# Performance work log

Measured on AMD Instinct MI355X. Metric: run time of the kernel, lower is better.

Reference implementation:

```python
import jax, jax.numpy as jnp
import numpy as np

V_SIZE, E, H = 30000, 256, 128   # vocab, emb_dim, GRU hidden per direction
B, U, T, ND = 32, 32, 128, 64    # dialogues, utterances, max tokens, dialogue-id table size
SCALE = E ** 0.5                  # attention normalise_factor = hid_size**0.5, hid_size = emb_dim


def _gru_dir(x_seq, w_ih, w_hh, b_ih, b_hh):
    """Unidirectional torch-style GRU. x_seq: [N,T,E] -> [N,T,H]."""
    xp = jnp.einsum('nte,ge->ntg', x_seq, w_ih) + b_ih   # precompute input gates [N,T,3H]
    xp = jnp.swapaxes(xp, 0, 1)                          # [T,N,3H]

    def step(h, xpt):
        gh = h @ w_hh.T + b_hh
        r = jax.nn.sigmoid(xpt[:, :H] + gh[:, :H])
        z = jax.nn.sigmoid(xpt[:, H:2 * H] + gh[:, H:2 * H])
        n = jnp.tanh(xpt[:, 2 * H:] + r * gh[:, 2 * H:])
        h_new = (1.0 - z) * n + z * h
        return h_new, h_new

    h0 = jnp.zeros((x_seq.shape[0], H), x_seq.dtype)
    _, out = jax.lax.scan(step, h0, xp)
    return jnp.swapaxes(out, 0, 1)


def _forward(x, d_ids, utt_len, emb_table,
             w_ih_f, w_hh_f, b_ih_f, b_hh_f,
             w_ih_b, w_hh_b, b_ih_b, b_hh_b,
             wq, bq, wk, bk, wv, bv, wo, bo, wl, bl):
    b, u, t = x.shape
    N = b * u
    emb = emb_table[x.reshape(N, t)]                      # [N,T,E]
    lens = jnp.clip(utt_len[d_ids].reshape(N), 1, t)      # valid tokens per utterance
    pos = jnp.arange(t)
    # index map that reverses the valid prefix (padding region clipped, unused)
    rev_idx = jnp.clip(lens[:, None] - 1 - pos[None, :], 0, t - 1)  # [N,T]

    o_f = _gru_dir(emb, w_ih_f, w_hh_f, b_ih_f, b_hh_f)   # causal => correct on valid prefix
    emb_rev = jnp.take_along_axis(emb, rev_idx[:, :, None], axis=1)
    o_b = jnp.take_along_axis(_gru_dir(emb_rev, w_ih_b, w_hh_b, b_ih_b, b_hh_b),
                              rev_idx[:, :, None], axis=1)
    h = jnp.concatenate([o_f, o_b], axis=-1)              # [N,T,E] bi-GRU states

    # self-attention pooling; original takes op[-1], so only the query at the
    # last valid token (lens-1) is needed -- identical math, less compute.
    k = jnp.einsum('nte,he->nth', h, wk) + bk
    v = jnp.einsum('nte,he->nth', h, wv) + bv
    h_last = jnp.take_along_axis(h, (lens - 1)[:, None, None], axis=1)[:, 0]  # [N,E]
    q = h_last @ wq.T + bq
    score = jnp.einsum('nh,nth->nt', q, k) / SCALE
    score = jnp.where(pos[None, :] < lens[:, None], score, -jnp.inf)
    attn = jax.nn.softmax(score, axis=-1)
    ctx = jnp.einsum('nt,nth->nh', attn, v)
    out = (ctx @ wo.T + bo) @ wl.T + bl                   # make_output then final linear
    return out.reshape(b, u, -1)


def setup_inputs() -> dict:
    key = jax.random.key(0)
    ks = jax.random.split(key, 16)

    def p(k, shape):
        return (jax.random.normal(k, shape, jnp.float32) / np.sqrt(shape[-1])).astype(jnp.float32)

    return {
        'x': jax.random.randint(ks[0], (B, U, T), 0, V_SIZE, dtype=jnp.int32),
        'd_ids': jax.random.randint(ks[1], (B,), 0, ND, dtype=jnp.int32),
        'utt_len': jax.random.randint(ks[2], (ND, U), 1, T + 1, dtype=jnp.int32),
        'emb_table': p(ks[3], (V_SIZE, E)),
        'w_ih_f': p(ks[4], (3 * H, E)), 'w_hh_f': p(ks[5], (3 * H, H)),
        'b_ih_f': jnp.zeros(3 * H, jnp.float32), 'b_hh_f': jnp.zeros(3 * H, jnp.float32),
        'w_ih_b': p(ks[6], (3 * H, E)), 'w_hh_b': p(ks[7], (3 * H, H)),
        'b_ih_b': jnp.zeros(3 * H, jnp.float32), 'b_hh_b': jnp.zeros(3 * H, jnp.float32),
        'wq': p(ks[8], (E, E)), 'bq': jnp.zeros(E, jnp.float32),
        'wk': p(ks[9], (E, E)), 'bk': jnp.zeros(E, jnp.float32),
        'wv': p(ks[10], (E, E)), 'bv': jnp.zeros(E, jnp.float32),
        'wo': p(ks[11], (E, E)), 'bo': jnp.zeros(E, jnp.float32),
        'wl': p(ks[12], (E, E)), 'bl': jnp.zeros(E, jnp.float32),
    }


def reference(x, d_ids, utt_len, emb_table,
              w_ih_f, w_hh_f, b_ih_f, b_hh_f,
              w_ih_b, w_hh_b, b_ih_b, b_hh_b,
              wq, bq, wk, bk, wv, bv, wo, bo, wl, bl):
    return _forward(x, d_ids, utt_len, emb_table,
                    w_ih_f, w_hh_f, b_ih_f, b_hh_f,
                    w_ih_b, w_hh_b, b_ih_b, b_hh_b,
                    wq, bq, wk, bk, wv, bv, wo, bo, wl, bl)
```

## Files before the change

### kernel.cpp

```cpp
#include <hip/hip_runtime.h>
#include <hip/hip_bf16.h>
#include <math.h>
#include <stdint.h>

typedef unsigned short u16;
typedef unsigned int   u32;
typedef __attribute__((ext_vector_type(8))) short bf16x8;
typedef __attribute__((ext_vector_type(4))) float f32x4;

#define EDIM 256
#define HDIM 128
#define TLEN 128
#define NUTT 1024
#define UU   32
#define NBU  8

#define WS_FLAG 0
#define WS_LENS 64
#define WS_TAB  4608
#define WS_COPY 8192
#define WS_OF   18874368LL
#define WS_OB   52428800LL

#define MFMA16(a, b, c) __builtin_amdgcn_mfma_f32_16x16x32_bf16((a), (b), (c), 0, 0, 0)
#define SOUT(u, s, j) ((u) * 1096 + (s) * 136 + (j))

__constant__ int G_SZ[18] = {7680000, 98304, 49152, 384, 384, 98304, 49152, 384, 384,
                             65536, 256, 65536, 65536, 256, 65536, 256, 65536, 256};

__device__ __forceinline__ float b2f(u16 b) {
    u32 u = ((u32)b) << 16; float f; __builtin_memcpy(&f, &u, 4); return f;
}
__device__ __forceinline__ u16 f2b(float f) {
    u32 u; __builtin_memcpy(&u, &f, 4);
    u32 r = u + 0x7FFFu + ((u >> 16) & 1u);
    return (u16)(r >> 16);
}
__device__ __forceinline__ u16 f2b_hw(float f) {
    __hip_bfloat16 h = __float2bfloat16(f);
    u16 v; __builtin_memcpy(&v, &h, 2); return v;
}
__device__ __forceinline__ float fsigmoid(float x) { return 1.0f / (1.0f + __expf(-x)); }
__device__ __forceinline__ float ftanh(float x) { return 1.0f - 2.0f / (__expf(2.0f * x) + 1.0f); }

__global__ __launch_bounds__(256)
void k_convert(void* ws,
               const int* __restrict__ d_ids, const int* __restrict__ utt_len,
               const void* a0, const void* a1, const void* a2, const void* a3,
               const void* a4, const void* a5, const void* a6, const void* a7,
               const void* a8, const void* a9, const void* a10, const void* a11,
               const void* a12, const void* a13, const void* a14, const void* a15,
               const void* a16, const void* a17) {
    __shared__ int scnt[4];
    const int tid = threadIdx.x, lane = tid & 63, wid = tid >> 6;
    const u16* p = (const u16*)a0;
    int cnt = 0;
#pragma unroll 8
    for (int i = tid; i < 16384; i += 256)
        cnt += ((p[i] & 0x7F80) == 0x7F80) ? 1 : 0;
#pragma unroll
    for (int o = 32; o > 0; o >>= 1) cnt += __shfl_down(cnt, o);
    if (lane == 0) scnt[wid] = cnt;
    __syncthreads();
    const int flag = (scnt[0] + scnt[1] + scnt[2] + scnt[3] > 0) ? 1 : 0;

    if (blockIdx.x == 0) {
        if (tid == 0) {
            const void* orig[18] = {a0,a1,a2,a3,a4,a5,a6,a7,a8,a9,a10,a11,a12,a13,a14,a15,a16,a17};
            *(int*)((char*)ws + WS_FLAG) = flag;
            const u16** tab = (const u16**)((char*)ws + WS_TAB);
            char* base = (char*)ws + WS_COPY;
            long long cum = 0;
            for (int a = 0; a < 18; ++a) {
                tab[a] = flag ? (const u16*)(base + cum * 2) : (const u16*)orig[a];
                cum += G_SZ[a];
            }
        }
        int* lens = (int*)((char*)ws + WS_LENS);
#pragma unroll 4
        for (int n = tid; n < NUTT; n += 256) {
            int b = n >> 5;
            int u = n & (UU - 1);
            int L = utt_len[d_ids[b] * UU + u];
            lens[n] = min(max(L, 1), TLEN);
        }
    }

    if (flag == 0) return;
    const void* orig[18] = {a0,a1,a2,a3,a4,a5,a6,a7,a8,a9,a10,a11,a12,a13,a14,a15,a16,a17};
    u16* base = (u16*)((char*)ws + WS_COPY);
    const int gtid = blockIdx.x * blockDim.x + tid;
    const int gs   = gridDim.x * blockDim.x;
    long long cum = 0;
    for (int a = 0; a < 18; ++a) {
        const float4* src = (const float4*)orig[a];
        uint2* dst = (uint2*)(base + cum);
        const int n4 = G_SZ[a] >> 2;
        for (int i = gtid; i < n4; i += gs) {
            float4 v = src[i];
            uint2 pk;
            pk.x = (u32)f2b(v.x) | ((u32)f2b(v.y) << 16);
            pk.y = (u32)f2b(v.z) | ((u32)f2b(v.w) << 16);
            dst[i] = pk;
        }
        cum += G_SZ[a];
    }
}

__global__ __launch_bounds__(512)
void k_scan(const int* __restrict__ x, void* ws) {
    const u16* const* tab = (const u16* const*)((char*)ws + WS_TAB);
    const int dir = blockIdx.y;
    const u16* emb  = tab[0];
    const u16* w_ih = tab[1 + dir * 4];
    const u16* w_hh = tab[2 + dir * 4];
    const u16* b_ih = tab[3 + dir * 4];
    const u16* b_hh = tab[4 + dir * 4];
    u16* outp = (u16*)((char*)ws + (dir ? WS_OB : WS_OF));
    const int* lens = (const int*)((char*)ws + WS_LENS);

    const int n0 = blockIdx.x * NBU;
    __shared__ __align__(16) u16 sh_emb[2][NBU][264];
    __shared__ __align__(16) u16 sh_hi[2][NBU * 136];
    __shared__ __align__(16) u16 sh_lo[2][NBU * 136];
    __shared__ __align__(16) u16 sh_out[2][NBU * 1096];
    __shared__ int sh_tok[NBU * 132];
    __shared__ int sh_L[NBU];

    const int tid = threadIdx.x, lane = tid & 63, wvi = tid >> 6;
    const int q4 = lane >> 4, mm = lane & 15;
    const int j = wvi * 16 + mm;
    const int u8 = mm & 7;
    const int arr0 = (q4 & 2);
    const bool a2 = (arr0 != 0);
    const bool lo32 = (lane < 32);

    for (int i = tid; i < NBU * 136; i += 512) { sh_hi[0][i] = 0; sh_lo[0][i] = 0; }
    for (int i = tid; i < NBU * TLEN; i += 512) {
        const int u = i >> 7, tt = i & 127;
        sh_tok[u * 132 + tt] = x[(n0 + u) * TLEN + tt];
    }
    if (tid < NBU) sh_L[tid] = lens[n0 + tid];

    bf16x8 wih[3][8]; bf16x8 whh[3][4];
    float bcr, bcz, bxn, bgn;
#pragma unroll
    for (int n3 = 0; n3 < 3; ++n3) {
        const int g = n3 * HDIM + j;
#pragma unroll
        for (int ks = 0; ks < 8; ++ks)
            wih[n3][ks] = *(const bf16x8*)(w_ih + g * EDIM + ks * 32 + q4 * 8);
#pragma unroll
        for (int ks = 0; ks < 4; ++ks)
            whh[n3][ks] = *(const bf16x8*)(w_hh + g * HDIM + ks * 32 + q4 * 8);
    }
    bcr = b2f(b_ih[j]) + b2f(b_hh[j]);
    bcz = b2f(b_ih[HDIM + j]) + b2f(b_hh[HDIM + j]);
    bxn = b2f(b_ih[2 * HDIM + j]);
    bgn = b2f(b_hh[2 * HDIM + j]);

    float hprev[2] = {0.f, 0.f};
    const f32x4 zero4 = {0.f, 0.f, 0.f, 0.f};
    __syncthreads();

    int Lm = sh_L[0];
#pragma unroll
    for (int u = 1; u < NBU; ++u) Lm = max(Lm, sh_L[u]);
    const int tmax = (Lm + 7) & ~7;

    const int pf_u = lane & 7;
    const int pf_c = (wvi & 3) * 8 + (lane >> 3);
    const int pf_L = sh_L[pf_u];
    const int tsel = wvi >> 2;

    {
        const int te = dir ? max(pf_L - 1 - tsel, 0) : tsel;
        const int tok = sh_tok[pf_u * 132 + te];
        uint4 v = *(const uint4*)(emb + (size_t)tok * EDIM + pf_c * 8);
        *(uint4*)&sh_emb[tsel][pf_u][pf_c * 8] = v;
    }
    __syncthreads();

    for (int t0 = 0; t0 < tmax; t0 += 2) {
        const int obuf = (t0 >> 3) & 1;
        const bool more = (t0 + 2 < tmax);

        uint4 pf;
        if (more) {
            const int tt = t0 + 2 + tsel;
            const int te = dir ? max(pf_L - 1 - tt, 0) : tt;
            const int tok = sh_tok[pf_u * 132 + te];
            pf = *(const uint4*)(emb + (size_t)tok * EDIM + pf_c * 8);
        }

        f32x4 accx[3];
        {
            const u16* eb_ = (mm < 8) ? &sh_emb[0][u8][0] : &sh_emb[1][u8][0];
            bf16x8 a = *(const bf16x8*)(eb_ + q4 * 8);
            accx[0] = MFMA16(a, wih[0][0], zero4);
            accx[1] = MFMA16(a, wih[1][0], zero4);
            accx[2] = MFMA16(a, wih[2][0], zero4);
#pragma unroll
            for (int ks = 1; ks < 8; ++ks) {
                bf16x8 av = *(const bf16x8*)(eb_ + ks * 32 + q4 * 8);
                accx[0] = MFMA16(av, wih[0][ks], accx[0]);
                accx[1] = MFMA16(av, wih[1][ks], accx[1]);
                accx[2] = MFMA16(av, wih[2][ks], accx[2]);
            }
        }
        float xA[3][2], xB[3][2];
#pragma unroll
        for (int g = 0; g < 3; ++g) {
#pragma unroll
            for (int r = 0; r < 2; ++r) {
                const float sv = a2 ? accx[g][r] : accx[g][2 + r];
                const float ov = a2 ? accx[g][2 + r] : accx[g][r];
                const float pv = __shfl_xor(sv, 32);
                xA[g][r] = lo32 ? ov : pv;
                xB[g][r] = lo32 ? pv : ov;
            }
        }

        {
            f32x4 accg[3];
            const u16* hb_ = ((mm < 8) ? sh_hi[0] : sh_lo[0]) + u8 * 136;
            {
                bf16x8 a = *(const bf16x8*)(hb_ + q4 * 8);
                accg[0] = MFMA16(a, whh[0][0], zero4);
                accg[1] = MFMA16(a, whh[1][0], zero4);
                accg[2] = MFMA16(a, whh[2][0], zero4);
            }
#pragma unroll
            for (int ks = 1; ks < 4; ++ks) {
                bf16x8 a = *(const bf16x8*)(hb_ + ks * 32 + q4 * 8);
                accg[0] = MFMA16(a, whh[0][ks], accg[0]);
                accg[1] = MFMA16(a, whh[1][ks], accg[1]);
                accg[2] = MFMA16(a, whh[2][ks], accg[2]);
            }
            const int slot = t0 & 7;
#pragma unroll
            for (int r = 0; r < 2; ++r) {
                float gg[3];
#pragma unroll
                for (int g = 0; g < 3; ++g) {
                    const float sv = a2 ? accg[g][r] : accg[g][2 + r];
                    const float ov = a2 ? accg[g][2 + r] : accg[g][r];
                    gg[g] = ov + __shfl_xor(sv, 32);
                }
                const int u = (q4 * 4 + arr0 + r) & 7;
                const float rg = fsigmoid(xA[0][r] + gg[0] + bcr);
                const float zg = fsigmoid(xA[1][r] + gg[1] + bcz);
                const float nn = ftanh((xA[2][r] + bxn) + rg * (gg[2] + bgn));
                const float hn = (1.0f - zg) * nn + zg * hprev[r];
                hprev[r] = hn;
                const u16 hb16 = f2b_hw(hn);
                sh_hi[1][u * 136 + j] = hb16;
                sh_lo[1][u * 136 + j] = f2b_hw(hn - b2f(hb16));
                sh_out[obuf][SOUT(u, slot, j)] = hb16;
            }
        }
        __syncthreads();

        {
            f32x4 accg[3];
            const u16* hb_ = ((mm < 8) ? sh_hi[1] : sh_lo[1]) + u8 * 136;
            {
                bf16x8 a = *(const bf16x8*)(hb_ + q4 * 8);
                accg[0] = MFMA16(a, whh[0][0], zero4);
                accg[1] = MFMA16(a, whh[1][0], zero4);
                accg[2] = MFMA16(a, whh[2][0], zero4);
            }
#pragma unroll
            for (int ks = 1; ks < 4; ++ks) {
                bf16x8 a = *(const bf16x8*)(hb_ + ks * 32 + q4 * 8);
                accg[0] = MFMA16(a, whh[0][ks], accg[0]);
                accg[1] = MFMA16(a, whh[1][ks], accg[1]);
                accg[2] = MFMA16(a, whh[2][ks], accg[2]);
            }
            const int slot = (t0 & 7) + 1;
#pragma unroll
            for (int r = 0; r < 2; ++r) {
                float gg[3];
#pragma unroll
                for (int g = 0; g < 3; ++g) {
                    const float sv = a2 ? accg[g][r] : accg[g][2 + r];
                    const float ov = a2 ? accg[g][2 + r] : accg[g][r];
                    gg[g] = ov + __shfl_xor(sv, 32);
                }
                const int u = (q4 * 4 + arr0 + r) & 7;
                const float rg = fsigmoid(xB[0][r] + gg[0] + bcr);
                const float zg = fsigmoid(xB[1][r] + gg[1] + bcz);
                const float nn = ftanh((xB[2][r] + bxn) + rg * (gg[2] + bgn));
                const float hn = (1.0f - zg) * nn + zg * hprev[r];
                hprev[r] = hn;
                const u16 hb16 = f2b_hw(hn);
                sh_hi[0][u * 136 + j] = hb16;
                sh_lo[0][u * 136 + j] = f2b_hw(hn - b2f(hb16));
                sh_out[obuf][SOUT(u, slot, j)] = hb16;
            }
        }
        if (more)
            *(uint4*)&sh_emb[tsel][pf_u][pf_c * 8] = pf;
        __syncthreads();

        if (((t0 + 1) & 7) == 7) {
            const int rowIdx = tid >> 3;
            const int part   = tid & 7;
            const int fu = rowIdx >> 3, fs = rowIdx & 7;
            const int tt = ((t0 + 1) & ~7) + fs;
            const int tout = dir ? (sh_L[fu] - 1 - tt) : tt;
            if (tout >= 0) {
                const u16* srcp = &sh_out[obuf][SOUT(fu, fs, part * 16)];
                uint4 v0 = *(const uint4*)(srcp);
                uint4 v1 = *(const uint4*)(srcp + 8);
                u16* dstp = outp + ((size_t)(n0 + fu) * TLEN + tout) * HDIM + part * 16;
                *(uint4*)(dstp)     = v0;
                *(uint4*)(dstp + 8) = v1;
            }
        }
    }
}

__global__ __launch_bounds__(256)
void k_attn(void* ws, void* outv) {
    const u16* const* tab = (const u16* const*)((char*)ws + WS_TAB);
    const u16* wq = tab[9];  const u16* bq = tab[10];
    const u16* wk = tab[11];
    const u16* wv = tab[12]; const u16* bv = tab[13];
    const u16* wo = tab[14]; const u16* bo = tab[15];
    const u16* wl = tab[16]; const u16* bl = tab[17];
    const int* lens = (const int*)((char*)ws + WS_LENS);
    const int flag = *(const int*)((const char*)ws + WS_FLAG);

    const int n = blockIdx.x;
    const int L = lens[n];
    const u16* hf = (const u16*)((char*)ws + WS_OF) + (size_t)n * TLEN * HDIM;
    const u16* hb = (const u16*)((char*)ws + WS_OB) + (size_t)n * TLEN * HDIM;

    __shared__ float sh_hl[EDIM];
    __shared__ float sh_v1[EDIM];
    __shared__ float sh_uv[EDIM];
    __shared__ float sh_a[4 * EDIM];
    __shared__ float sh_m[4], sh_l[4];

    const int tid = threadIdx.x, lane = tid & 63, wid = tid >> 6;

    sh_hl[tid] = (tid < HDIM) ? b2f(hf[(size_t)(L - 1) * HDIM + tid])
                              : b2f(hb[(size_t)(L - 1) * HDIM + (tid - HDIM)]);
    __syncthreads();

    {
        float s0 = b2f(bq[tid]), s1 = 0.0f;
        const u16* wr = wq + tid * EDIM;
#pragma unroll
        for (int ks = 0; ks < 32; ks += 2) {
            bf16x8 w8 = *(const bf16x8*)(wr + ks * 8);
            bf16x8 w9 = *(const bf16x8*)(wr + ks * 8 + 8);
#pragma unroll
            for (int d = 0; d < 8; ++d) {
                s0 += b2f((u16)w8[d]) * sh_hl[ks * 8 + d];
                s1 += b2f((u16)w9[d]) * sh_hl[ks * 8 + 8 + d];
            }
        }
        sh_v1[tid] = s0 + s1;
    }
    __syncthreads();

    {
        float s0 = 0.0f, s1 = 0.0f;
        for (int i = 0; i < EDIM; i += 2) {
            s0 += b2f(wk[i * EDIM + tid]) * sh_v1[i];
            s1 += b2f(wk[(i + 1) * EDIM + tid]) * sh_v1[i + 1];
        }
        sh_uv[tid] = s0 + s1;
    }
    __syncthreads();

    {
        const int e0 = lane * 4;
        const float u0 = sh_uv[e0], u1 = sh_uv[e0 + 1];
        const float u2 = sh_uv[e0 + 2], u3 = sh_uv[e0 + 3];
        float m = -1e30f, l = 0.0f;
        float a0 = 0.f, a1 = 0.f, a2 = 0.f, a3 = 0.f;
        for (int t = wid; t < L; t += 4) {
            const u16* src = (lane < 32) ? (hf + (size_t)t * HDIM + lane * 4)
                                         : (hb + (size_t)t * HDIM + (lane - 32) * 4);
            uint2 pv = *(const uint2*)src;
            const float h0 = b2f((u16)(pv.x & 0xFFFF));
            const float h1 = b2f((u16)(pv.x >> 16));
            const float h2 = b2f((u16)(pv.y & 0xFFFF));
            const float h3 = b2f((u16)(pv.y >> 16));
            float p = h0 * u0 + h1 * u1 + h2 * u2 + h3 * u3;
#pragma unroll
            for (int o = 32; o > 0; o >>= 1) p += __shfl_xor(p, o);
            const float s = p * 0.0625f;
            const float mn = fmaxf(m, s);
            const float c = __expf(m - mn);
            const float w = __expf(s - mn);
            l = l * c + w;
            a0 = a0 * c + w * h0;
            a1 = a1 * c + w * h1;
            a2 = a2 * c + w * h2;
            a3 = a3 * c + w * h3;
            m = mn;
        }
        sh_a[wid * EDIM + e0]     = a0;
        sh_a[wid * EDIM + e0 + 1] = a1;
        sh_a[wid * EDIM + e0 + 2] = a2;
        sh_a[wid * EDIM + e0 + 3] = a3;
        if (lane == 0) { sh_m[wid] = m; sh_l[wid] = l; }
    }
    __syncthreads();

    {
        const float m0 = sh_m[0], m1 = sh_m[1], m2 = sh_m[2], m3 = sh_m[3];
        const float M = fmaxf(fmaxf(m0, m1), fmaxf(m2, m3));
        const float c0 = __expf(m0 - M), c1 = __expf(m1 - M);
        const float c2 = __expf(m2 - M), c3 = __expf(m3 - M);
        const float den = c0 * sh_l[0] + c1 * sh_l[1] + c2 * sh_l[2] + c3 * sh_l[3];
        const float num = c0 * sh_a[tid] + c1 * sh_a[EDIM + tid] +
                          c2 * sh_a[2 * EDIM + tid] + c3 * sh_a[3 * EDIM + tid];
        sh_hl[tid] = num / den;
    }
    __syncthreads();

    {
        float s0 = b2f(bv[tid]), s1 = 0.0f;
        const u16* wr = wv + tid * EDIM;
#pragma unroll
        for (int ks = 0; ks < 32; ks += 2) {
            bf16x8 w8 = *(const bf16x8*)(wr + ks * 8);
            bf16x8 w9 = *(const bf16x8*)(wr + ks * 8 + 8);
#pragma unroll
            for (int d = 0; d < 8; ++d) {
                s0 += b2f((u16)w8[d]) * sh_hl[ks * 8 + d];
                s1 += b2f((u16)w9[d]) * sh_hl[ks * 8 + 8 + d];
            }
        }
        sh_uv[tid] = s0 + s1;
    }
    __syncthreads();

    {
        float s0 = b2f(bo[tid]), s1 = 0.0f;
        const u16* wr = wo + tid * EDIM;
#pragma unroll
        for (int ks = 0; ks < 32; ks += 2) {
            bf16x8 w8 = *(const bf16x8*)(wr + ks * 8);
            bf16x8 w9 = *(const bf16x8*)(wr + ks * 8 + 8);
#pragma unroll
            for (int d = 0; d < 8; ++d) {
                s0 += b2f((u16)w8[d]) * sh_uv[ks * 8 + d];
                s1 += b2f((u16)w9[d]) * sh_uv[ks * 8 + 8 + d];
            }
        }
        sh_v1[tid] = s0 + s1;
    }
    __syncthreads();

    {
        float s0 = b2f(bl[tid]), s1 = 0.0f;
        const u16* wr = wl + tid * EDIM;
#pragma unroll
        for (int ks = 0; ks < 32; ks += 2) {
            bf16x8 w8 = *(const bf16x8*)(wr + ks * 8);
            bf16x8 w9 = *(const bf16x8*)(wr + ks * 8 + 8);
#pragma unroll
            for (int d = 0; d < 8; ++d) {
                s0 += b2f((u16)w8[d]) * sh_v1[ks * 8 + d];
                s1 += b2f((u16)w9[d]) * sh_v1[ks * 8 + 8 + d];
            }
        }
        const float s = s0 + s1;
        const size_t oidx = (size_t)n * EDIM + tid;
        if (flag) ((float*)outv)[oidx] = s;
        else      ((u16*)outv)[oidx]   = f2b(s);
    }
}

extern "C" void kernel_launch(void* const* d_in, const int* in_sizes, int n_in,
                              void* d_out, int out_size, void* d_ws, size_t ws_size,
                              hipStream_t stream) {
    const int* x       = (const int*)d_in[0];
    const int* d_ids   = (const int*)d_in[1];
    const int* utt_len = (const int*)d_in[2];
    const void* f_arr[18] = {
        d_in[3],
        d_in[4], d_in[5], d_in[6], d_in[7],
        d_in[8], d_in[9], d_in[10], d_in[11],
        d_in[12], d_in[13],
        d_in[14],
        d_in[16], d_in[17],
        d_in[18], d_in[19],
        d_in[20], d_in[21]
    };

    k_convert<<<512, 256, 0, stream>>>(d_ws, d_ids, utt_len,
        f_arr[0], f_arr[1], f_arr[2], f_arr[3], f_arr[4], f_arr[5], f_arr[6], f_arr[7],
        f_arr[8], f_arr[9], f_arr[10], f_arr[11], f_arr[12], f_arr[13], f_arr[14],
        f_arr[15], f_arr[16], f_arr[17]);

    k_scan<<<dim3(NUTT / NBU, 2), 512, 0, stream>>>(x, d_ws);

    k_attn<<<NUTT, 256, 0, stream>>>(d_ws, d_out);
}
```

Baseline: 370.5 us.

## Software-pipeline GRU input projection one step ahead, interleaved with recurrent MFMAs

The GRU scan kernel now computes the input-gate MFMA projection for the next pair of timesteps during the current pair's recurrent matmuls. It splits the eight k-steps across the two recurrent phases and double-buffers the embedding staging in shared memory (two pairs of slots), prefetching two steps further ahead. This takes the input projection off the serial critical path of the recurrence, at the cost of more shared memory and more live registers. It also adds an unroll pragma to a key-projection loop in the attention kernel.

Result: slower. 380.9 us (+2.8%).

```diff
diff --git a/kernel.cpp b/kernel.cpp
--- a/kernel.cpp
+++ b/kernel.cpp
@@ -42,6 +42,8 @@
 }
 __device__ __forceinline__ float fsigmoid(float x) { return 1.0f / (1.0f + __expf(-x)); }
 __device__ __forceinline__ float ftanh(float x) { return 1.0f - 2.0f / (__expf(2.0f * x) + 1.0f); }
+
+__device__ __forceinline__ float xor32f(float v) { return __shfl_xor(v, 32); }
 
 __global__ __launch_bounds__(256)
 void k_convert(void* ws,
@@ -120,7 +122,7 @@
     const int* lens = (const int*)((char*)ws + WS_LENS);
 
     const int n0 = blockIdx.x * NBU;
-    __shared__ __align__(16) u16 sh_emb[2][NBU][264];
+    __shared__ __align__(16) u16 sh_emb[4][NBU][264];
     __shared__ __align__(16) u16 sh_hi[2][NBU * 136];
     __shared__ __align__(16) u16 sh_lo[2][NBU * 136];
     __shared__ __align__(16) u16 sh_out[2][NBU * 1096];
@@ -174,40 +176,48 @@
     const int tsel = wvi >> 2;
 
     {
-        const int te = dir ? max(pf_L - 1 - tsel, 0) : tsel;
-        const int tok = sh_tok[pf_u * 132 + te];
-        uint4 v = *(const uint4*)(emb + (size_t)tok * EDIM + pf_c * 8);
-        *(uint4*)&sh_emb[tsel][pf_u][pf_c * 8] = v;
-    }
-    __syncthreads();
+#pragma unroll
+        for (int pp = 0; pp < 2; ++pp) {
+            const int tt = 2 * pp + tsel;
+            const int te = dir ? max(pf_L - 1 - tt, 0) : tt;
+            const int tok = sh_tok[pf_u * 132 + te];
+            uint4 v = *(const uint4*)(emb + (size_t)tok * EDIM + pf_c * 8);
+            *(uint4*)&sh_emb[pp * 2 + tsel][pf_u][pf_c * 8] = v;
+        }
+    }
+    __syncthreads();
+
+    f32x4 accx[3];
+    {
+        const u16* eb_ = (mm < 8) ? &sh_emb[0][u8][0] : &sh_emb[1][u8][0];
+        bf16x8 a = *(const bf16x8*)(eb_ + q4 * 8);
+        accx[0] = MFMA16(a, wih[0][0], zero4);
+        accx[1] = MFMA16(a, wih[1][0], zero4);
+        accx[2] = MFMA16(a, wih[2][0], zero4);
+#pragma unroll
+        for (int ks = 1; ks < 8; ++ks) {
+            bf16x8 av = *(const bf16x8*)(eb_ + ks * 32 + q4 * 8);
+            accx[0] = MFMA16(av, wih[0][ks], accx[0]);
+            accx[1] = MFMA16(av, wih[1][ks], accx[1]);
+            accx[2] = MFMA16(av, wih[2][ks], accx[2]);
+        }
+    }
 
     for (int t0 = 0; t0 < tmax; t0 += 2) {
-        const int obuf = (t0 >> 3) & 1;
-        const bool more = (t0 + 2 < tmax);
+        const int pr  = (t0 >> 1) & 1;
+        const int prn = pr ^ 1;
+        const int obuf = (t0 >> 3) & 1, slot = t0 & 7;
+        const bool morex = (t0 + 2 < tmax);
+        const bool stg   = (t0 + 4 < tmax);
 
         uint4 pf;
-        if (more) {
-            const int tt = t0 + 2 + tsel;
+        if (stg) {
+            const int tt = t0 + 4 + tsel;
             const int te = dir ? max(pf_L - 1 - tt, 0) : tt;
             const int tok = sh_tok[pf_u * 132 + te];
             pf = *(const uint4*)(emb + (size_t)tok * EDIM + pf_c * 8);
         }
 
-        f32x4 accx[3];
-        {
-            const u16* eb_ = (mm < 8) ? &sh_emb[0][u8][0] : &sh_emb[1][u8][0];
-            bf16x8 a = *(const bf16x8*)(eb_ + q4 * 8);
-            accx[0] = MFMA16(a, wih[0][0], zero4);
-            accx[1] = MFMA16(a, wih[1][0], zero4);
-            accx[2] = MFMA16(a, wih[2][0], zero4);
-#pragma unroll
-            for (int ks = 1; ks < 8; ++ks) {
-                bf16x8 av = *(const bf16x8*)(eb_ + ks * 32 + q4 * 8);
-                accx[0] = MFMA16(av, wih[0][ks], accx[0]);
-                accx[1] = MFMA16(av, wih[1][ks], accx[1]);
-                accx[2] = MFMA16(av, wih[2][ks], accx[2]);
-            }
-        }
         float xA[3][2], xB[3][2];
 #pragma unroll
         for (int g = 0; g < 3; ++g) {
@@ -215,11 +225,14 @@
             for (int r = 0; r < 2; ++r) {
                 const float sv = a2 ? accx[g][r] : accx[g][2 + r];
                 const float ov = a2 ? accx[g][2 + r] : accx[g][r];
-                const float pv = __shfl_xor(sv, 32);
+                const float pv = xor32f(sv);
                 xA[g][r] = lo32 ? ov : pv;
                 xB[g][r] = lo32 ? pv : ov;
             }
         }
+
+        const u16* ebn = (mm < 8) ? &sh_emb[prn * 2][u8][0]
+                                  : &sh_emb[prn * 2 + 1][u8][0];
 
         {
             f32x4 accg[3];
@@ -237,7 +250,19 @@
                 accg[1] = MFMA16(a, whh[1][ks], accg[1]);
                 accg[2] = MFMA16(a, whh[2][ks], accg[2]);
             }
-            const int slot = t0 & 7;
+            if (morex) {
+                bf16x8 a = *(const bf16x8*)(ebn + q4 * 8);
+                accx[0] = MFMA16(a, wih[0][0], zero4);
+                accx[1] = MFMA16(a, wih[1][0], zero4);
+                accx[2] = MFMA16(a, wih[2][0], zero4);
+#pragma unroll
+                for (int ks = 1; ks < 4; ++ks) {
+                    bf16x8 av = *(const bf16x8*)(ebn + ks * 32 + q4 * 8);
+                    accx[0] = MFMA16(av, wih[0][ks], accx[0]);
+                    accx[1] = MFMA16(av, wih[1][ks], accx[1]);
+                    accx[2] = MFMA16(av, wih[2][ks], accx[2]);
+                }
+            }
 #pragma unroll
             for (int r = 0; r < 2; ++r) {
                 float gg[3];
@@ -245,7 +270,7 @@
                 for (int g = 0; g < 3; ++g) {
                     const float sv = a2 ? accg[g][r] : accg[g][2 + r];
                     const float ov = a2 ? accg[g][2 + r] : accg[g][r];
-                    gg[g] = ov + __shfl_xor(sv, 32);
+                    gg[g] = ov + xor32f(sv);
                 }
                 const int u = (q4 * 4 + arr0 + r) & 7;
                 const float rg = fsigmoid(xA[0][r] + gg[0] + bcr);
@@ -277,7 +302,16 @@
                 accg[1] = MFMA16(a, whh[1][ks], accg[1]);
                 accg[2] = MFMA16(a, whh[2][ks], accg[2]);
             }
-            const int slot = (t0 & 7) + 1;
+            if (morex) {
+#pragma unroll
+                for (int ks = 4; ks < 8; ++ks) {
+                    bf16x8 av = *(const bf16x8*)(ebn + ks * 32 + q4 * 8);
+                    accx[0] = MFMA16(av, wih[0][ks], accx[0]);
+                    accx[1] = MFMA16(av, wih[1][ks], accx[1]);
+                    accx[2] = MFMA16(av, wih[2][ks], accx[2]);
+                }
+            }
+            const int slot1 = slot + 1;
 #pragma unroll
             for (int r = 0; r < 2; ++r) {
                 float gg[3];
@@ -285,7 +319,7 @@
                 for (int g = 0; g < 3; ++g) {
                     const float sv = a2 ? accg[g][r] : accg[g][2 + r];
                     const float ov = a2 ? accg[g][2 + r] : accg[g][r];
-                    gg[g] = ov + __shfl_xor(sv, 32);
+                    gg[g] = ov + xor32f(sv);
                 }
                 const int u = (q4 * 4 + arr0 + r) & 7;
                 const float rg = fsigmoid(xB[0][r] + gg[0] + bcr);
@@ -296,11 +330,11 @@
                 const u16 hb16 = f2b_hw(hn);
                 sh_hi[0][u * 136 + j] = hb16;
                 sh_lo[0][u * 136 + j] = f2b_hw(hn - b2f(hb16));
-                sh_out[obuf][SOUT(u, slot, j)] = hb16;
-            }
-        }
-        if (more)
-            *(uint4*)&sh_emb[tsel][pf_u][pf_c * 8] = pf;
+                sh_out[obuf][SOUT(u, slot1, j)] = hb16;
+            }
+        }
+        if (stg)
+            *(uint4*)&sh_emb[pr * 2 + tsel][pf_u][pf_c * 8] = pf;
         __syncthreads();
 
         if (((t0 + 1) & 7) == 7) {
@@ -368,6 +402,7 @@
 
     {
         float s0 = 0.0f, s1 = 0.0f;
+#pragma unroll 8
         for (int i = 0; i < EDIM; i += 2) {
             s0 += b2f(wk[i * EDIM + tid]) * sh_v1[i];
             s1 += b2f(wk[(i + 1) * EDIM + tid]) * sh_v1[i + 1];
```
